# Performance work log

Measured on AMD Instinct MI355X. Metric: run time of the kernel, lower is better.

## Reference

```python
import jax, jax.numpy as jnp
import numpy as np

B, L, F, R = 32, 128, 128, 4096
MAX_INTERIOR = R >> 1  # tpr.max_interior_index
N = 262144


def setup_inputs() -> dict:
    key = jax.random.key(0)
    ks = jax.random.split(key, 7)
    mem_values = jax.random.normal(ks[0], (N, F), dtype=jnp.float32)
    # zero out a slice of rows so the ConsNet pad_mask path is exercised
    mem_values = mem_values.at[: N // 20].set(0.0)
    arg_weights = jax.random.uniform(ks[1], (B, L, 4), dtype=jnp.float32)
    root_filler = jax.random.normal(ks[2], (B, F), dtype=jnp.float32)
    op_dist = jax.random.uniform(ks[3], (B, 3), dtype=jnp.float32)
    batch_idx = jax.random.randint(ks[4], (N,), 0, B, dtype=jnp.int32)
    slot_idx = jax.random.randint(ks[5], (N,), 0, L, dtype=jnp.int32)
    role_idx = jax.random.randint(ks[6], (N,), 0, R, dtype=jnp.int32)
    return {
        "mem_values": mem_values,
        "arg_weights": arg_weights,
        "root_filler": root_filler,
        "op_dist": op_dist,
        "batch_idx": batch_idx,
        "slot_idx": slot_idx,
        "role_idx": role_idx,
    }


def _forward(mem_values, arg_weights, root_filler, op_dist,
             batch_idx, slot_idx, role_idx):
    # per-entry gather of the 4 argument weights: w[n,k] = arg_weights[b_n, l_n, k]
    w = arg_weights[batch_idx, slot_idx]  # [N, 4]
    flat = batch_idx.astype(jnp.int32) * R + role_idx  # [N], coalesce key (b, r)

    def coalesce(vals):  # scatter-add == torch_sparse.coalesce into dense [B,R,F]
        g = jnp.zeros((B * R, F), vals.dtype).at[flat].add(vals)
        return g.reshape(B, R, F)

    H = R >> 1

    # ---- CarNet (sparse): weight, coalesce, keep even roles, role >>= 1 ----
    car_A = coalesce(mem_values * w[:, 0:1])            # [B,R,F]
    car_out = jnp.zeros((B, R, F), mem_values.dtype).at[:, :H].set(car_A[:, 0::2])

    # ---- CdrNet (sparse): keep odd roles != 1, role >>= 1 ----
    cdr_A = coalesce(mem_values * w[:, 1:2])
    cdr_half = cdr_A[:, 1::2]                            # roles 2r+1 -> r
    cdr_half = cdr_half.at[:, 0].set(0.0)                # exclude old role 1 (r=0)
    cdr_out = jnp.zeros((B, R, F), mem_values.dtype).at[:, :H].set(cdr_half)

    # ---- ConsNet (sparse): pad-mask weights, roles<MAX_INTERIOR, children + root ----
    pad = jnp.all(mem_values == 0, axis=1, keepdims=True)  # [N,1]
    c1 = coalesce(mem_values * jnp.where(pad, 0.0, w[:, 2:3]))
    c2 = coalesce(mem_values * jnp.where(pad, 0.0, w[:, 3:4]))
    cons_out = jnp.zeros((B, R, F), mem_values.dtype)
    cons_out = cons_out.at[:, 0::2].set(c1[:, :MAX_INTERIOR])      # r -> 2r
    cons_out = cons_out.at[:, 1::2].add(c2[:, :MAX_INTERIOR])      # r -> 2r+1
    cons_out = cons_out.at[:, 1].add(root_filler)                  # root at role 1

    # ---- op-distribution weighted combine (coalesce of the 3 streams) ----
    out = (op_dist[:, 0, None, None] * car_out
           + op_dist[:, 1, None, None] * cdr_out
           + op_dist[:, 2, None, None] * cons_out)
    return out


def reference(mem_values, arg_weights, root_filler, op_dist,
              batch_idx, slot_idx, role_idx):
    return _forward(mem_values, arg_weights, root_filler, op_dist,
                    batch_idx, slot_idx, role_idx)
```

## Files before the change

kernel.cpp:

```cpp
#include <hip/hip_runtime.h>


namespace {
constexpr int kB = 32;
constexpr int kL = 128;
constexpr int kF = 128;
constexpr int kR = 4096;
constexpr int kN = 262144;
constexpr int kQ = 2048;
constexpr int kNP = kB * kQ;
constexpr int kCap = 16;
constexpr int kOvfMax = 65536;

constexpr size_t kOffRowCnt  = 0;
constexpr size_t kOffConsCnt = 262144;
constexpr size_t kOffOvfCnt  = 524288;
constexpr size_t kOffOvf     = 524304;
constexpr size_t kOffRowEnt  = 1572880;
constexpr size_t kOffConsEnt = 9961488;
}

__global__ __launch_bounds__(256) void build_kernel(
    const float4* __restrict__ aw, const float* __restrict__ opd,
    const int* __restrict__ bidx, const int* __restrict__ sidx,
    const int* __restrict__ ridx,
    int* __restrict__ rowcnt, int* __restrict__ conscnt,
    int* __restrict__ ovf_cnt, int4* __restrict__ ovf,
    int2* __restrict__ rowent, int4* __restrict__ consent) {
  int n = blockIdx.x * 256 + threadIdx.x;
  if (n >= kN) return;
  int b = bidx[n];
  int s = sidx[n];
  int rr = ridx[n];
  float4 w = aw[b * kL + s];
  float op0 = opd[3 * b + 0];
  float op1 = opd[3 * b + 1];
  float op2 = opd[3 * b + 2];

  bool even = (rr & 1) == 0;
  if (even || rr >= 3) {
    float sc = even ? op0 * w.x : op1 * w.y;
    int key = (b << 11) | (rr >> 1);
    int pos = atomicAdd(&rowcnt[key], 1);
    if (pos < kCap) {
      rowent[key * kCap + pos] = make_int2(n, __float_as_int(sc));
    } else {
      int o = atomicAdd(ovf_cnt, 1);
      if (o < kOvfMax)
        ovf[o] = make_int4(b * kR + (rr >> 1), n, __float_as_int(sc), 0);
    }
  }
  if (rr < kQ) {
    int key = (b << 11) | rr;
    int pos = atomicAdd(&conscnt[key], 1);
    if (pos < kCap) {
      consent[key * kCap + pos] =
          make_int4(n, __float_as_int(op2 * w.z), __float_as_int(op2 * w.w), 0);
    } else {
      int o = atomicAdd(ovf_cnt, 2);
      if (o < kOvfMax)
        ovf[o] = make_int4(b * kR + 2 * rr, n, __float_as_int(op2 * w.z), 0);
      if (o + 1 < kOvfMax)
        ovf[o + 1] =
            make_int4(b * kR + 2 * rr + 1, n, __float_as_int(op2 * w.w), 0);
    }
  }
}

__global__ __launch_bounds__(256) void gather_kernel(
    const float2* __restrict__ mem2, const float2* __restrict__ root2,
    const float* __restrict__ opd,
    const int* __restrict__ rowcnt, const int* __restrict__ conscnt,
    const int2* __restrict__ rowent, const int2* __restrict__ consent2,
    float2* __restrict__ out2) {
  const int p = blockIdx.x * 4 + (threadIdx.x >> 6);
  const int t = threadIdx.x & 63;
  const int b = p >> 11;
  const int q = p & (kQ - 1);
  const bool hashalf = q < 1024;

  int cn_raw = conscnt[p];
  int2 ce = make_int2(0, 0);
  if (t < 32) ce = (consent2 + (size_t)p * 2 * kCap)[t];
  int2 hc = make_int2(0, 0);
  int2 he = make_int2(0, 0);
  if (hashalf) {
    int key0 = (b << 11) | (q << 1);
    hc = *(const int2*)(rowcnt + key0);
    if (t < 32) he = (rowent + (size_t)key0 * kCap)[t];
  }
  int cn = min(__builtin_amdgcn_readfirstlane(cn_raw), kCap);
  int h0 = 0, h1 = 0;
  if (hashalf) {
    h0 = min(__builtin_amdgcn_readfirstlane(hc.x), kCap);
    h1 = min(__builtin_amdgcn_readfirstlane(hc.y), kCap);
  }

  float2 mc[4];
  float c1s[4], c2s[4];
#pragma unroll
  for (int j = 0; j < 4; ++j) {
    c1s[j] = 0.f;
    c2s[j] = 0.f;
    mc[j] = make_float2(0.f, 0.f);
  }
  if (cn > 0) {
#pragma unroll
    for (int j = 0; j < 4; ++j) {
      bool v = j < cn;
      int nn = __shfl(ce.x, 2 * j);
      float a = __int_as_float(__shfl(ce.y, 2 * j));
      float bb = __int_as_float(__shfl(ce.x, 2 * j + 1));
      nn = v ? nn : 0;
      c1s[j] = v ? a : 0.f;
      c2s[j] = v ? bb : 0.f;
      mc[j] = mem2[(size_t)nn * (kF / 2) + t];
    }
  }
  float2 m0[8], m1[8];
  float s0a[8], s1a[8];
#pragma unroll
  for (int j = 0; j < 8; ++j) {
    s0a[j] = 0.f;
    s1a[j] = 0.f;
    m0[j] = make_float2(0.f, 0.f);
    m1[j] = make_float2(0.f, 0.f);
  }
  if (h0 > 0) {
#pragma unroll
    for (int j = 0; j < 4; ++j) {
      bool v = j < h0;
      int nn = __shfl(he.x, j);
      float s = __int_as_float(__shfl(he.y, j));
      nn = v ? nn : 0;
      s0a[j] = v ? s : 0.f;
      m0[j] = mem2[(size_t)nn * (kF / 2) + t];
    }
    if (h0 > 4) {
#pragma unroll
      for (int j = 4; j < 8; ++j) {
        bool v = j < h0;
        int nn = __shfl(he.x, j);
        float s = __int_as_float(__shfl(he.y, j));
        nn = v ? nn : 0;
        s0a[j] = v ? s : 0.f;
        m0[j] = mem2[(size_t)nn * (kF / 2) + t];
      }
    }
  }
  if (h1 > 0) {
#pragma unroll
    for (int j = 0; j < 4; ++j) {
      bool v = j < h1;
      int nn = __shfl(he.x, 16 + j);
      float s = __int_as_float(__shfl(he.y, 16 + j));
      nn = v ? nn : 0;
      s1a[j] = v ? s : 0.f;
      m1[j] = mem2[(size_t)nn * (kF / 2) + t];
    }
    if (h1 > 4) {
#pragma unroll
      for (int j = 4; j < 8; ++j) {
        bool v = j < h1;
        int nn = __shfl(he.x, 16 + j);
        float s = __int_as_float(__shfl(he.y, 16 + j));
        nn = v ? nn : 0;
        s1a[j] = v ? s : 0.f;
        m1[j] = mem2[(size_t)nn * (kF / 2) + t];
      }
    }
  }

  float ax0 = 0.f, ay0 = 0.f, ax1 = 0.f, ay1 = 0.f;
#pragma unroll
  for (int j = 0; j < 4; ++j) {
    ax0 += c1s[j] * mc[j].x;
    ay0 += c1s[j] * mc[j].y;
    ax1 += c2s[j] * mc[j].x;
    ay1 += c2s[j] * mc[j].y;
  }
#pragma unroll
  for (int j = 0; j < 8; ++j) {
    ax0 += s0a[j] * m0[j].x;
    ay0 += s0a[j] * m0[j].y;
  }
#pragma unroll
  for (int j = 0; j < 8; ++j) {
    ax1 += s1a[j] * m1[j].x;
    ay1 += s1a[j] * m1[j].y;
  }

  for (int i = 4; i < cn; i += 4) {
#pragma unroll
    for (int j = 0; j < 4; ++j) {
      int idx = i + j;
      bool v = idx < cn;
      int nn = __shfl(ce.x, 2 * idx);
      float a = __int_as_float(__shfl(ce.y, 2 * idx));
      float bb = __int_as_float(__shfl(ce.x, 2 * idx + 1));
      nn = v ? nn : 0;
      a = v ? a : 0.f;
      bb = v ? bb : 0.f;
      float2 m = mem2[(size_t)nn * (kF / 2) + t];
      ax0 += a * m.x;
      ay0 += a * m.y;
      ax1 += bb * m.x;
      ay1 += bb * m.y;
    }
  }
  for (int i = 8; i < h0; i += 4) {
#pragma unroll
    for (int j = 0; j < 4; ++j) {
      int idx = i + j;
      bool v = idx < h0;
      int nn = __shfl(he.x, idx);
      float s = __int_as_float(__shfl(he.y, idx));
      nn = v ? nn : 0;
      s = v ? s : 0.f;
      float2 m = mem2[(size_t)nn * (kF / 2) + t];
      ax0 += s * m.x;
      ay0 += s * m.y;
    }
  }
  for (int i = 8; i < h1; i += 4) {
#pragma unroll
    for (int j = 0; j < 4; ++j) {
      int idx = i + j;
      bool v = idx < h1;
      int nn = __shfl(he.x, 16 + idx);
      float s = __int_as_float(__shfl(he.y, 16 + idx));
      nn = v ? nn : 0;
      s = v ? s : 0.f;
      float2 m = mem2[(size_t)nn * (kF / 2) + t];
      ax1 += s * m.x;
      ay1 += s * m.y;
    }
  }

  if (q == 0) {
    float op2 = opd[3 * b + 2];
    float2 rf = root2[b * (kF / 2) + t];
    ax1 += op2 * rf.x;
    ay1 += op2 * rf.y;
  }
  size_t orow = ((size_t)b * kR + 2 * q) * (kF / 2) + t;
  out2[orow] = make_float2(ax0, ay0);
  out2[orow + (kF / 2)] = make_float2(ax1, ay1);
}

__global__ __launch_bounds__(128) void ovf_kernel(
    const float* __restrict__ mem, const int* __restrict__ ovf_cnt,
    const int4* __restrict__ ovf, float* __restrict__ out) {
  int m = *ovf_cnt;
  if (m > kOvfMax) m = kOvfMax;
  const int t = threadIdx.x;
  for (int i = blockIdx.x; i < m; i += gridDim.x) {
    int4 e = ovf[i];
    float sc = __int_as_float(e.z);
    atomicAdd(&out[(size_t)e.x * kF + t], sc * mem[(size_t)e.y * kF + t]);
  }
}

extern "C" void kernel_launch(void* const* d_in, const int* in_sizes, int n_in,
                              void* d_out, int out_size, void* d_ws, size_t ws_size,
                              hipStream_t stream) {
  const float* mem   = (const float*)d_in[0];
  const float* aw    = (const float*)d_in[1];
  const float* rootf = (const float*)d_in[2];
  const float* opd   = (const float*)d_in[3];
  const int* bidx    = (const int*)d_in[4];
  const int* sidx    = (const int*)d_in[5];
  const int* ridx    = (const int*)d_in[6];

  char* ws = (char*)d_ws;
  int* rowcnt   = (int*)(ws + kOffRowCnt);
  int* conscnt  = (int*)(ws + kOffConsCnt);
  int* ovf_cnt  = (int*)(ws + kOffOvfCnt);
  int4* ovf     = (int4*)(ws + kOffOvf);
  int2* rowent  = (int2*)(ws + kOffRowEnt);
  int4* consent = (int4*)(ws + kOffConsEnt);

  hipMemsetAsync(ws, 0, kOffOvfCnt + 16, stream);

  build_kernel<<<kN / 256, 256, 0, stream>>>(
      (const float4*)aw, opd, bidx, sidx, ridx, rowcnt, conscnt, ovf_cnt, ovf,
      rowent, consent);

  gather_kernel<<<kNP / 4, 256, 0, stream>>>(
      (const float2*)mem, (const float2*)rootf, opd, rowcnt, conscnt, rowent,
      (const int2*)consent, (float2*)d_out);

  ovf_kernel<<<64, 128, 0, stream>>>(mem, ovf_cnt, ovf, (float*)d_out);
}
```

Baseline: 272.5 us.

## Process four output row-pairs per wavefront to batch gather loads

Result: no change. 268.8 us (-1.3%).

```diff
diff --git a/kernel.cpp b/kernel.cpp
--- a/kernel.cpp
+++ b/kernel.cpp
@@ -67,185 +67,168 @@
   }
 }
 
+#define CONS_ISSUE(M, CE, BASE, CNT)                     \
+  _Pragma("unroll") for (int j = 0; j < 4; ++j) {        \
+    int nn = __shfl((CE).x, (BASE) + 2 * j);             \
+    nn = (j < (CNT)) ? nn : 0;                           \
+    M[j] = mem2[(size_t)nn * 64 + t];                    \
+  }
+
+#define HALF_ISSUE(M, HE, BASE, CNT)                     \
+  if ((CNT) > 0) {                                       \
+    _Pragma("unroll") for (int j = 0; j < 4; ++j) {      \
+      int nn = __shfl((HE).x, (BASE) + j);               \
+      nn = (j < (CNT)) ? nn : 0;                         \
+      M[j] = mem2[(size_t)nn * 64 + t];                  \
+    }                                                    \
+    if ((CNT) > 4) {                                     \
+      _Pragma("unroll") for (int j = 4; j < 8; ++j) {    \
+        int nn = __shfl((HE).x, (BASE) + j);             \
+        nn = (j < (CNT)) ? nn : 0;                       \
+        M[j] = mem2[(size_t)nn * 64 + t];                \
+      }                                                  \
+    }                                                    \
+  }
+
+#define CONS_ACC(M, CE, BASE, CNT)                                     \
+  _Pragma("unroll") for (int j = 0; j < 4; ++j) {                      \
+    bool v = j < (CNT);                                                \
+    float a = __int_as_float(__shfl((CE).y, (BASE) + 2 * j));          \
+    float bb = __int_as_float(__shfl((CE).x, (BASE) + 2 * j + 1));     \
+    a = v ? a : 0.f;                                                   \
+    bb = v ? bb : 0.f;                                                 \
+    ax0 += a * M[j].x;                                                 \
+    ay0 += a * M[j].y;                                                 \
+    ax1 += bb * M[j].x;                                                \
+    ay1 += bb * M[j].y;                                                \
+  }                                                                    \
+  for (int ii = 4; ii < (CNT); ii += 4) {   \
+    _Pragma("unroll") for (int j = 0; j < 4; ++j) {                    \
+      int idx = ii + j;                                                \
+      bool v = idx < (CNT);                                            \
+      int nn = __shfl((CE).x, (BASE) + 2 * idx);                       \
+      float a = __int_as_float(__shfl((CE).y, (BASE) + 2 * idx));      \
+      float bb = __int_as_float(__shfl((CE).x, (BASE) + 2 * idx + 1)); \
+      nn = v ? nn : 0;                                                 \
+      a = v ? a : 0.f;                                                 \
+      bb = v ? bb : 0.f;                                               \
+      float2 m = mem2[(size_t)nn * 64 + t];                            \
+      ax0 += a * m.x;                                                  \
+      ay0 += a * m.y;                                                  \
+      ax1 += bb * m.x;                                                 \
+      ay1 += bb * m.y;                                                 \
+    }                                                                  \
+  }
+
+#define HALF_ACC(M, HE, BASE, CNT, AX, AY)                             \
+  _Pragma("unroll") for (int j = 0; j < 8; ++j) {                      \
+    bool v = j < (CNT);                                                \
+    float s = __int_as_float(__shfl((HE).y, (BASE) + j));              \
+    s = v ? s : 0.f;                                                   \
+    AX += s * M[j].x;                                                  \
+    AY += s * M[j].y;                                                  \
+  }                                                                    \
+  for (int ii = 8; ii < (CNT); ii += 4) {   \
+    _Pragma("unroll") for (int j = 0; j < 4; ++j) {                    \
+      int idx = ii + j;                                                \
+      bool v = idx < (CNT);                                            \
+      int nn = __shfl((HE).x, (BASE) + idx);                           \
+      float s = __int_as_float(__shfl((HE).y, (BASE) + idx));          \
+      nn = v ? nn : 0;                                                 \
+      s = v ? s : 0.f;                                                 \
+      float2 m = mem2[(size_t)nn * 64 + t];                            \
+      AX += s * m.x;                                                   \
+      AY += s * m.y;                                                   \
+    }                                                                  \
+  }
+
 __global__ __launch_bounds__(256) void gather_kernel(
     const float2* __restrict__ mem2, const float2* __restrict__ root2,
     const float* __restrict__ opd,
     const int* __restrict__ rowcnt, const int* __restrict__ conscnt,
-    const int2* __restrict__ rowent, const int2* __restrict__ consent2,
+    const int2* __restrict__ rowent2, const int2* __restrict__ consent2,
     float2* __restrict__ out2) {
-  const int p = blockIdx.x * 4 + (threadIdx.x >> 6);
+  const int wv = blockIdx.x * 4 + (threadIdx.x >> 6);
   const int t = threadIdx.x & 63;
-  const int b = p >> 11;
-  const int q = p & (kQ - 1);
-  const bool hashalf = q < 1024;
-
-  int cn_raw = conscnt[p];
-  int2 ce = make_int2(0, 0);
-  if (t < 32) ce = (consent2 + (size_t)p * 2 * kCap)[t];
-  int2 hc = make_int2(0, 0);
-  int2 he = make_int2(0, 0);
-  if (hashalf) {
-    int key0 = (b << 11) | (q << 1);
-    hc = *(const int2*)(rowcnt + key0);
-    if (t < 32) he = (rowent + (size_t)key0 * kCap)[t];
-  }
-  int cn = min(__builtin_amdgcn_readfirstlane(cn_raw), kCap);
-  int h0 = 0, h1 = 0;
-  if (hashalf) {
-    h0 = min(__builtin_amdgcn_readfirstlane(hc.x), kCap);
-    h1 = min(__builtin_amdgcn_readfirstlane(hc.y), kCap);
-  }
-
-  float2 mc[4];
-  float c1s[4], c2s[4];
-#pragma unroll
-  for (int j = 0; j < 4; ++j) {
-    c1s[j] = 0.f;
-    c2s[j] = 0.f;
-    mc[j] = make_float2(0.f, 0.f);
-  }
-  if (cn > 0) {
-#pragma unroll
-    for (int j = 0; j < 4; ++j) {
-      bool v = j < cn;
-      int nn = __shfl(ce.x, 2 * j);
-      float a = __int_as_float(__shfl(ce.y, 2 * j));
-      float bb = __int_as_float(__shfl(ce.x, 2 * j + 1));
-      nn = v ? nn : 0;
-      c1s[j] = v ? a : 0.f;
-      c2s[j] = v ? bb : 0.f;
-      mc[j] = mem2[(size_t)nn * (kF / 2) + t];
-    }
-  }
-  float2 m0[8], m1[8];
-  float s0a[8], s1a[8];
+  const int b = wv >> 9;
+  const int i = wv & 511;
+  const int plo = (b << 11) | (2 * i);
+  const int phi = plo + 1024;
+  const int kb4 = (b << 11) | (4 * i);
+
+  const int2 cnlo = *(const int2*)(conscnt + plo);
+  const int2 cnhi = *(const int2*)(conscnt + phi);
+  const int4 hc4 = *(const int4*)(rowcnt + kb4);
+  const int2 ceL = consent2[(size_t)plo * 32 + t];
+  const int2 ceH = consent2[(size_t)phi * 32 + t];
+  const int2 he = rowent2[(size_t)kb4 * 16 + t];
+
+  const int cn0 = min(__builtin_amdgcn_readfirstlane(cnlo.x), kCap);
+  const int cn1 = min(__builtin_amdgcn_readfirstlane(cnlo.y), kCap);
+  const int cn2 = min(__builtin_amdgcn_readfirstlane(cnhi.x), kCap);
+  const int cn3 = min(__builtin_amdgcn_readfirstlane(cnhi.y), kCap);
+  const int h00 = min(__builtin_amdgcn_readfirstlane(hc4.x), kCap);
+  const int h01 = min(__builtin_amdgcn_readfirstlane(hc4.y), kCap);
+  const int h10 = min(__builtin_amdgcn_readfirstlane(hc4.z), kCap);
+  const int h11 = min(__builtin_amdgcn_readfirstlane(hc4.w), kCap);
+
+  float2 mcA[4], mcB[4], mcC[4], mcD[4];
+  float2 m0A[8], m1A[8], m0B[8], m1B[8];
 #pragma unroll
   for (int j = 0; j < 8; ++j) {
-    s0a[j] = 0.f;
-    s1a[j] = 0.f;
-    m0[j] = make_float2(0.f, 0.f);
-    m1[j] = make_float2(0.f, 0.f);
-  }
-  if (h0 > 0) {
-#pragma unroll
-    for (int j = 0; j < 4; ++j) {
-      bool v = j < h0;
-      int nn = __shfl(he.x, j);
-      float s = __int_as_float(__shfl(he.y, j));
-      nn = v ? nn : 0;
-      s0a[j] = v ? s : 0.f;
-      m0[j] = mem2[(size_t)nn * (kF / 2) + t];
+    m0A[j] = make_float2(0.f, 0.f);
+    m1A[j] = make_float2(0.f, 0.f);
+    m0B[j] = make_float2(0.f, 0.f);
+    m1B[j] = make_float2(0.f, 0.f);
+  }
+
+  CONS_ISSUE(mcA, ceL, 0, cn0);
+  CONS_ISSUE(mcB, ceL, 32, cn1);
+  CONS_ISSUE(mcC, ceH, 0, cn2);
+  CONS_ISSUE(mcD, ceH, 32, cn3);
+  HALF_ISSUE(m0A, he, 0, h00);
+  HALF_ISSUE(m1A, he, 16, h01);
+  HALF_ISSUE(m0B, he, 32, h10);
+  HALF_ISSUE(m1B, he, 48, h11);
+
+  {
+    float ax0 = 0.f, ay0 = 0.f, ax1 = 0.f, ay1 = 0.f;
+    CONS_ACC(mcA, ceL, 0, cn0);
+    HALF_ACC(m0A, he, 0, h00, ax0, ay0);
+    HALF_ACC(m1A, he, 16, h01, ax1, ay1);
+    if ((plo & (kQ - 1)) == 0) {
+      float op2 = opd[3 * b + 2];
+      float2 rf = root2[b * 64 + t];
+      ax1 += op2 * rf.x;
+      ay1 += op2 * rf.y;
     }
-    if (h0 > 4) {
-#pragma unroll
-      for (int j = 4; j < 8; ++j) {
-        bool v = j < h0;
-        int nn = __shfl(he.x, j);
-        float s = __int_as_float(__shfl(he.y, j));
-        nn = v ? nn : 0;
-        s0a[j] = v ? s : 0.f;
-        m0[j] = mem2[(size_t)nn * (kF / 2) + t];
-      }
-    }
-  }
-  if (h1 > 0) {
-#pragma unroll
-    for (int j = 0; j < 4; ++j) {
-      bool v = j < h1;
-      int nn = __shfl(he.x, 16 + j);
-      float s = __int_as_float(__shfl(he.y, 16 + j));
-      nn = v ? nn : 0;
-      s1a[j] = v ? s : 0.f;
-      m1[j] = mem2[(size_t)nn * (kF / 2) + t];
-    }
-    if (h1 > 4) {
-#pragma unroll
-      for (int j = 4; j < 8; ++j) {
-        bool v = j < h1;
-        int nn = __shfl(he.x, 16 + j);
-        float s = __int_as_float(__shfl(he.y, 16 + j));
-        nn = v ? nn : 0;
-        s1a[j] = v ? s : 0.f;
-        m1[j] = mem2[(size_t)nn * (kF / 2) + t];
-      }
-    }
-  }
-
-  float ax0 = 0.f, ay0 = 0.f, ax1 = 0.f, ay1 = 0.f;
-#pragma unroll
-  for (int j = 0; j < 4; ++j) {
-    ax0 += c1s[j] * mc[j].x;
-    ay0 += c1s[j] * mc[j].y;
-    ax1 += c2s[j] * mc[j].x;
-    ay1 += c2s[j] * mc[j].y;
-  }
-#pragma unroll
-  for (int j = 0; j < 8; ++j) {
-    ax0 += s0a[j] * m0[j].x;
-    ay0 += s0a[j] * m0[j].y;
-  }
-#pragma unroll
-  for (int j = 0; j < 8; ++j) {
-    ax1 += s1a[j] * m1[j].x;
-    ay1 += s1a[j] * m1[j].y;
-  }
-
-  for (int i = 4; i < cn; i += 4) {
-#pragma unroll
-    for (int j = 0; j < 4; ++j) {
-      int idx = i + j;
-      bool v = idx < cn;
-      int nn = __shfl(ce.x, 2 * idx);
-      float a = __int_as_float(__shfl(ce.y, 2 * idx));
-      float bb = __int_as_float(__shfl(ce.x, 2 * idx + 1));
-      nn = v ? nn : 0;
-      a = v ? a : 0.f;
-      bb = v ? bb : 0.f;
-      float2 m = mem2[(size_t)nn * (kF / 2) + t];
-      ax0 += a * m.x;
-      ay0 += a * m.y;
-      ax1 += bb * m.x;
-      ay1 += bb * m.y;
-    }
-  }
-  for (int i = 8; i < h0; i += 4) {
-#pragma unroll
-    for (int j = 0; j < 4; ++j) {
-      int idx = i + j;
-      bool v = idx < h0;
-      int nn = __shfl(he.x, idx);
-      float s = __int_as_float(__shfl(he.y, idx));
-      nn = v ? nn : 0;
-      s = v ? s : 0.f;
-      float2 m = mem2[(size_t)nn * (kF / 2) + t];
-      ax0 += s * m.x;
-      ay0 += s * m.y;
-    }
-  }
-  for (int i = 8; i < h1; i += 4) {
-#pragma unroll
-    for (int j = 0; j < 4; ++j) {
-      int idx = i + j;
-      bool v = idx < h1;
-      int nn = __shfl(he.x, 16 + idx);
-      float s = __int_as_float(__shfl(he.y, 16 + idx));
-      nn = v ? nn : 0;
-      s = v ? s : 0.f;
-      float2 m = mem2[(size_t)nn * (kF / 2) + t];
-      ax1 += s * m.x;
-      ay1 += s * m.y;
-    }
-  }
-
-  if (q == 0) {
-    float op2 = opd[3 * b + 2];
-    float2 rf = root2[b * (kF / 2) + t];
-    ax1 += op2 * rf.x;
-    ay1 += op2 * rf.y;
-  }
-  size_t orow = ((size_t)b * kR + 2 * q) * (kF / 2) + t;
-  out2[orow] = make_float2(ax0, ay0);
-  out2[orow + (kF / 2)] = make_float2(ax1, ay1);
+    size_t orow = (size_t)plo * 128 + t;
+    out2[orow] = make_float2(ax0, ay0);
+    out2[orow + 64] = make_float2(ax1, ay1);
+  }
+  {
+    float ax0 = 0.f, ay0 = 0.f, ax1 = 0.f, ay1 = 0.f;
+    CONS_ACC(mcB, ceL, 32, cn1);
+    HALF_ACC(m0B, he, 32, h10, ax0, ay0);
+    HALF_ACC(m1B, he, 48, h11, ax1, ay1);
+    size_t orow = (size_t)(plo + 1) * 128 + t;
+    out2[orow] = make_float2(ax0, ay0);
+    out2[orow + 64] = make_float2(ax1, ay1);
+  }
+  {
+    float ax0 = 0.f, ay0 = 0.f, ax1 = 0.f, ay1 = 0.f;
+    CONS_ACC(mcC, ceH, 0, cn2);
+    size_t orow = (size_t)phi * 128 + t;
+    out2[orow] = make_float2(ax0, ay0);
+    out2[orow + 64] = make_float2(ax1, ay1);
+  }
+  {
+    float ax0 = 0.f, ay0 = 0.f, ax1 = 0.f, ay1 = 0.f;
+    CONS_ACC(mcD, ceH, 32, cn3);
+    size_t orow = (size_t)(phi + 1) * 128 + t;
+    out2[orow] = make_float2(ax0, ay0);
+    out2[orow + 64] = make_float2(ax1, ay1);
+  }
 }
 
 __global__ __launch_bounds__(128) void ovf_kernel(
@@ -286,9 +269,9 @@
       (const float4*)aw, opd, bidx, sidx, ridx, rowcnt, conscnt, ovf_cnt, ovf,
       rowent, consent);
 
-  gather_kernel<<<kNP / 4, 256, 0, stream>>>(
-      (const float2*)mem, (const float2*)rootf, opd, rowcnt, conscnt, rowent,
-      (const int2*)consent, (float2*)d_out);
+  gather_kernel<<<kNP / 16, 256, 0, stream>>>(
+      (const float2*)mem, (const float2*)rootf, opd, rowcnt, conscnt,
+      (const int2*)rowent, (const int2*)consent, (float2*)d_out);
 
   ovf_kernel<<<64, 128, 0, stream>>>(mem, ovf_cnt, ovf, (float*)d_out);
 }
```
